# Performance work log

Hardware: AMD Instinct MI355X
Metric: run time of the kernel (lower is better)

The kernel has to match this reference:

```python
import jax, jax.numpy as jnp
import numpy as np

MEX_C = 2.0 / (np.sqrt(3.0) * np.pi ** 0.25)

def mexican_hat(z):
    return MEX_C * (z * z - 1.0) * jnp.exp(-0.5 * z * z)

def setup_inputs() -> dict:
    key = jax.random.key(0)
    ks = jax.random.split(key, 5)
    B, T, D, O = 4, 2048, 128, 128
    x = jax.random.normal(ks[0], (B, T, D), dtype=jnp.float32)
    # init like torch: scale ~ U(0.5,1.5), translation ~ U(-0.5,0.5), kaiming-ish weights
    scale = jax.random.uniform(ks[1], (O, D), dtype=jnp.float32, minval=0.5, maxval=1.5)
    translation = jax.random.uniform(ks[2], (O, D), dtype=jnp.float32, minval=-0.5, maxval=0.5)
    bound = 1.0 / np.sqrt(D)
    wavelet_weights = jax.random.uniform(ks[3], (O, D), dtype=jnp.float32, minval=-bound, maxval=bound)
    base_w = jax.random.uniform(ks[4], (O, D), dtype=jnp.float32, minval=-bound, maxval=bound)
    ln_gamma = jnp.ones((D,), dtype=jnp.float32)
    ln_beta = jnp.zeros((D,), dtype=jnp.float32)
    return {"x": x, "scale": scale, "translation": translation,
            "wavelet_weights": wavelet_weights, "base_w": base_w,
            "ln_gamma": ln_gamma, "ln_beta": ln_beta}

def reference(x, scale, translation, wavelet_weights, base_w, ln_gamma, ln_beta):
    B, T, D = x.shape
    O = wavelet_weights.shape[0]
    # LayerNorm over last dim (eps = 1e-5, torch default)
    mu = jnp.mean(x, axis=-1, keepdims=True)
    var = jnp.mean((x - mu) ** 2, axis=-1, keepdims=True)
    x_norm = (x - mu) / jnp.sqrt(var + 1e-5) * ln_gamma + ln_beta
    x_flat = x_norm.reshape(B * T, D)                      # (N, D)
    s = jax.nn.softplus(scale) + 0.1                       # (O, D)
    # broadcast intermediate (N, O, D) — the memory-bound path
    z = (x_flat[:, None, :] - translation[None]) / s[None]
    w = jnp.clip(mexican_hat(z), -10.0, 10.0)              # (N, O, D)
    wavelet_out = jnp.einsum('nod,od->no', w, wavelet_weights)
    base_out = x.reshape(B * T, D) @ base_w.T              # base uses raw x
    out = wavelet_out + jax.nn.silu(base_out)
    return out.reshape(B, T, O)
```

## Files before the change

kernel.cpp:

```cpp
#include <hip/hip_runtime.h>


#define D_DIM 128
#define O_DIM 128
#define ROWS  16
#define BLOCK 1024
#define CHUNK 16
#define NCHUNK (D_DIM / CHUNK)
#define XSTRIDE 9

#define C1     0.72134752f
#define SQRT_C 0.84932180f
#define WWK    1.2023651f
#define LOG2E  1.44269504f

typedef float v2f __attribute__((ext_vector_type(2)));

__global__ __launch_bounds__(256) void wavekan_prep(
    const float* __restrict__ scale,
    const float* __restrict__ trans,
    const float* __restrict__ ww,
    const float* __restrict__ bw,
    float4* __restrict__ wsW)
{
    int idx = blockIdx.x * blockDim.x + threadIdx.x;
    if (idx >= O_DIM * D_DIM) return;
    int o = idx >> 7;
    int d = idx & (D_DIM - 1);
    float sc = scale[idx];
    float sp = fmaxf(sc, 0.0f) + log1pf(__expf(-fabsf(sc)));
    float is2 = SQRT_C / (sp + 0.1f);
    float4 w;
    w.x = trans[idx] * is2;
    w.y = is2;
    w.z = ww[idx] * WWK;
    w.w = bw[idx];
    wsW[d * O_DIM + o] = w;
}

template<bool USE_WS>
__global__ __launch_bounds__(BLOCK, 8) void wavekan_main(
    const float* __restrict__ x,
    const float* __restrict__ scale,
    const float* __restrict__ trans,
    const float* __restrict__ ww,
    const float* __restrict__ bw,
    const float* __restrict__ gamma,
    const float* __restrict__ beta,
    const float4* __restrict__ wsW,
    float* __restrict__ out,
    int N)
{
    __shared__ float4 s_x[D_DIM * XSTRIDE];
    __shared__ float4 s_w[CHUNK * O_DIM];

    const int tid  = threadIdx.x;
    const int row0 = blockIdx.x * ROWS;

    {
        const int r  = tid >> 6;
        const int j  = tid & 63;
        const int d0 = j * 2;
        const int grow = row0 + r;

        float2 v2 = make_float2(0.f, 0.f);
        if (grow < N)
            v2 = *reinterpret_cast<const float2*>(x + (size_t)grow * D_DIM + d0);

        float sum = v2.x + v2.y;
        float ssq = v2.x * v2.x + v2.y * v2.y;
        #pragma unroll
        for (int m = 1; m < 64; m <<= 1) {
            sum += __shfl_xor(sum, m, 64);
            ssq += __shfl_xor(ssq, m, 64);
        }
        const float mean = sum * (1.0f / D_DIM);
        const float var  = ssq * (1.0f / D_DIM) - mean * mean;
        const float rstd = rsqrtf(var + 1e-5f);

        float2 g2 = *reinterpret_cast<const float2*>(gamma + d0);
        float2 b2 = *reinterpret_cast<const float2*>(beta + d0);

        const int p  = r >> 1;
        const int h  = r & 1;
        float* c0 = reinterpret_cast<float*>(&s_x[d0 * XSTRIDE + p]);
        float* c1 = reinterpret_cast<float*>(&s_x[(d0 + 1) * XSTRIDE + p]);
        c0[h]     = (v2.x - mean) * rstd * g2.x + b2.x;
        c0[2 + h] = v2.x;
        c1[h]     = (v2.y - mean) * rstd * g2.y + b2.y;
        c1[2 + h] = v2.y;
    }

    const int o = tid & (O_DIM - 1);
    const int g = tid >> 7;

    v2f accw = {0.f, 0.f};
    v2f accb = {0.f, 0.f};

    if (USE_WS) {
        float4 r0 = wsW[tid];
        float4 r1 = wsW[tid + BLOCK];
        for (int c = 0; c < NCHUNK; ++c) {
            __syncthreads();
            s_w[tid]         = r0;
            s_w[tid + BLOCK] = r1;
            if (c + 1 < NCHUNK) {
                r0 = wsW[(c + 1) * (CHUNK * O_DIM) + tid];
                r1 = wsW[(c + 1) * (CHUNK * O_DIM) + tid + BLOCK];
            }
            __syncthreads();

            #pragma unroll
            for (int dl = 0; dl < CHUNK; ++dl) {
                float4 w  = s_w[dl * O_DIM + o];
                float4 xx = s_x[(c * CHUNK + dl) * XSTRIDE + g];
                v2f xln = {xx.x, xx.y};
                v2f xrw = {xx.z, xx.w};
                v2f u   = xln * w.y - w.x;
                v2f q   = u * u;
                v2f s1  = q - C1;
                v2f e   = {__builtin_amdgcn_exp2f(-q.x),
                           __builtin_amdgcn_exp2f(-q.y)};
                accw += (s1 * e) * w.z;
                accb += xrw * w.w;
            }
        }
    } else {
        __syncthreads();
        for (int d = 0; d < D_DIM; ++d) {
            int idx = o * D_DIM + d;
            float sc = scale[idx];
            float sp = fmaxf(sc, 0.0f) + log1pf(__expf(-fabsf(sc)));
            float is  = SQRT_C / (sp + 0.1f);
            float tws = trans[idx] * is;
            float wwk = ww[idx] * WWK;
            float bwv = bw[idx];
            float4 xx = s_x[d * XSTRIDE + g];
            v2f xln = {xx.x, xx.y};
            v2f xrw = {xx.z, xx.w};
            v2f u   = xln * is - tws;
            v2f q   = u * u;
            v2f s1  = q - C1;
            v2f e   = {__builtin_amdgcn_exp2f(-q.x),
                       __builtin_amdgcn_exp2f(-q.y)};
            accw += (s1 * e) * wwk;
            accb += xrw * bwv;
        }
    }

    {
        const int rr0 = row0 + g * 2;
        if (rr0 < N) {
            float sig0 = 1.0f / (1.0f + __builtin_amdgcn_exp2f(-LOG2E * accb.x));
            out[(size_t)rr0 * O_DIM + o] = accw.x + accb.x * sig0;
        }
        if (rr0 + 1 < N) {
            float sig1 = 1.0f / (1.0f + __builtin_amdgcn_exp2f(-LOG2E * accb.y));
            out[(size_t)(rr0 + 1) * O_DIM + o] = accw.y + accb.y * sig1;
        }
    }
}

extern "C" void kernel_launch(void* const* d_in, const int* in_sizes, int n_in,
                              void* d_out, int out_size, void* d_ws, size_t ws_size,
                              hipStream_t stream) {
    const float* x     = (const float*)d_in[0];
    const float* scale = (const float*)d_in[1];
    const float* trans = (const float*)d_in[2];
    const float* ww    = (const float*)d_in[3];
    const float* bw    = (const float*)d_in[4];
    const float* gamma = (const float*)d_in[5];
    const float* beta  = (const float*)d_in[6];
    float* out = (float*)d_out;

    const int N = in_sizes[0] / D_DIM;
    const int grid = (N + ROWS - 1) / ROWS;

    const size_t ws_needed = (size_t)O_DIM * D_DIM * sizeof(float4);
    if (ws_size >= ws_needed) {
        wavekan_prep<<<(O_DIM * D_DIM + 255) / 256, 256, 0, stream>>>(
            scale, trans, ww, bw, (float4*)d_ws);
        wavekan_main<true><<<grid, BLOCK, 0, stream>>>(
            x, scale, trans, ww, bw, gamma, beta, (const float4*)d_ws, out, N);
    } else {
        wavekan_main<false><<<grid, BLOCK, 0, stream>>>(
            x, scale, trans, ww, bw, gamma, beta, nullptr, out, N);
    }
}
```

Before: 97.29 us.

## Fuse weight preprocessing into main kernel and drop separate prep launch

Removes the separate prep kernel that wrote transformed per-(o,d) parameters to workspace. Each block now loads the raw scale, translation and weights chunk by chunk, computes the softplus-derived terms in registers, and transposes them into shared memory, with the next chunk's loads and transform overlapped with compute. This saves a kernel launch and a workspace round trip. In exchange every block (512 of them) recomputes log1p/exp/div for the whole weight set, and the shared-memory store becomes strided.

```diff
diff --git a/kernel.cpp b/kernel.cpp
--- a/kernel.cpp
+++ b/kernel.cpp
@@ -16,29 +16,17 @@
 
 typedef float v2f __attribute__((ext_vector_type(2)));
 
-__global__ __launch_bounds__(256) void wavekan_prep(
-    const float* __restrict__ scale,
-    const float* __restrict__ trans,
-    const float* __restrict__ ww,
-    const float* __restrict__ bw,
-    float4* __restrict__ wsW)
-{
-    int idx = blockIdx.x * blockDim.x + threadIdx.x;
-    if (idx >= O_DIM * D_DIM) return;
-    int o = idx >> 7;
-    int d = idx & (D_DIM - 1);
-    float sc = scale[idx];
-    float sp = fmaxf(sc, 0.0f) + log1pf(__expf(-fabsf(sc)));
+__device__ __forceinline__ float4 wk_transform(float sc, float tr, float w_w, float b_w) {
+    float sp  = fmaxf(sc, 0.0f) + log1pf(__expf(-fabsf(sc)));
     float is2 = SQRT_C / (sp + 0.1f);
     float4 w;
-    w.x = trans[idx] * is2;
+    w.x = tr * is2;
     w.y = is2;
-    w.z = ww[idx] * WWK;
-    w.w = bw[idx];
-    wsW[d * O_DIM + o] = w;
+    w.z = w_w * WWK;
+    w.w = b_w;
+    return w;
 }
 
-template<bool USE_WS>
 __global__ __launch_bounds__(BLOCK, 8) void wavekan_main(
     const float* __restrict__ x,
     const float* __restrict__ scale,
@@ -47,7 +35,6 @@
     const float* __restrict__ bw,
     const float* __restrict__ gamma,
     const float* __restrict__ beta,
-    const float4* __restrict__ wsW,
     float* __restrict__ out,
     int N)
 {
@@ -91,60 +78,60 @@
         c1[2 + h] = v2.y;
     }
 
+    const int so    = tid >> 3;
+    const int sq    = tid & 7;
+    const int wbase = so * D_DIM + sq * 2;
+
+    float4 r0, r1;
+    {
+        float2 sc2 = *reinterpret_cast<const float2*>(scale + wbase);
+        float2 tr2 = *reinterpret_cast<const float2*>(trans + wbase);
+        float2 wv2 = *reinterpret_cast<const float2*>(ww    + wbase);
+        float2 bv2 = *reinterpret_cast<const float2*>(bw    + wbase);
+        r0 = wk_transform(sc2.x, tr2.x, wv2.x, bv2.x);
+        r1 = wk_transform(sc2.y, tr2.y, wv2.y, bv2.y);
+    }
+
     const int o = tid & (O_DIM - 1);
     const int g = tid >> 7;
 
     v2f accw = {0.f, 0.f};
     v2f accb = {0.f, 0.f};
 
-    if (USE_WS) {
-        float4 r0 = wsW[tid];
-        float4 r1 = wsW[tid + BLOCK];
-        for (int c = 0; c < NCHUNK; ++c) {
-            __syncthreads();
-            s_w[tid]         = r0;
-            s_w[tid + BLOCK] = r1;
-            if (c + 1 < NCHUNK) {
-                r0 = wsW[(c + 1) * (CHUNK * O_DIM) + tid];
-                r1 = wsW[(c + 1) * (CHUNK * O_DIM) + tid + BLOCK];
-            }
-            __syncthreads();
+    for (int c = 0; c < NCHUNK; ++c) {
+        __syncthreads();
+        s_w[(sq * 2)     * O_DIM + so] = r0;
+        s_w[(sq * 2 + 1) * O_DIM + so] = r1;
+        __syncthreads();
 
-            #pragma unroll
-            for (int dl = 0; dl < CHUNK; ++dl) {
-                float4 w  = s_w[dl * O_DIM + o];
-                float4 xx = s_x[(c * CHUNK + dl) * XSTRIDE + g];
-                v2f xln = {xx.x, xx.y};
-                v2f xrw = {xx.z, xx.w};
-                v2f u   = xln * w.y - w.x;
-                v2f q   = u * u;
-                v2f s1  = q - C1;
-                v2f e   = {__builtin_amdgcn_exp2f(-q.x),
-                           __builtin_amdgcn_exp2f(-q.y)};
-                accw += (s1 * e) * w.z;
-                accb += xrw * w.w;
-            }
+        float2 sc2, tr2, wv2, bv2;
+        const bool more = (c + 1 < NCHUNK);
+        if (more) {
+            const int off = wbase + (c + 1) * CHUNK;
+            sc2 = *reinterpret_cast<const float2*>(scale + off);
+            tr2 = *reinterpret_cast<const float2*>(trans + off);
+            wv2 = *reinterpret_cast<const float2*>(ww    + off);
+            bv2 = *reinterpret_cast<const float2*>(bw    + off);
         }
-    } else {
-        __syncthreads();
-        for (int d = 0; d < D_DIM; ++d) {
-            int idx = o * D_DIM + d;
-            float sc = scale[idx];
-            float sp = fmaxf(sc, 0.0f) + log1pf(__expf(-fabsf(sc)));
-            float is  = SQRT_C / (sp + 0.1f);
-            float tws = trans[idx] * is;
-            float wwk = ww[idx] * WWK;
-            float bwv = bw[idx];
-            float4 xx = s_x[d * XSTRIDE + g];
+
+        #pragma unroll
+        for (int dl = 0; dl < CHUNK; ++dl) {
+            float4 w  = s_w[dl * O_DIM + o];
+            float4 xx = s_x[(c * CHUNK + dl) * XSTRIDE + g];
             v2f xln = {xx.x, xx.y};
             v2f xrw = {xx.z, xx.w};
-            v2f u   = xln * is - tws;
+            v2f u   = xln * w.y - w.x;
             v2f q   = u * u;
             v2f s1  = q - C1;
             v2f e   = {__builtin_amdgcn_exp2f(-q.x),
                        __builtin_amdgcn_exp2f(-q.y)};
-            accw += (s1 * e) * wwk;
-            accb += xrw * bwv;
+            accw += (s1 * e) * w.z;
+            accb += xrw * w.w;
+        }
+
+        if (more) {
+            r0 = wk_transform(sc2.x, tr2.x, wv2.x, bv2.x);
+            r1 = wk_transform(sc2.y, tr2.y, wv2.y, bv2.y);
         }
     }
 
@@ -176,14 +163,8 @@
     const int N = in_sizes[0] / D_DIM;
     const int grid = (N + ROWS - 1) / ROWS;
 
-    const size_t ws_needed = (size_t)O_DIM * D_DIM * sizeof(float4);
-    if (ws_size >= ws_needed) {
-        wavekan_prep<<<(O_DIM * D_DIM + 255) / 256, 256, 0, stream>>>(
-            scale, trans, ww, bw, (float4*)d_ws);
-        wavekan_main<true><<<grid, BLOCK, 0, stream>>>(
-            x, scale, trans, ww, bw, gamma, beta, (const float4*)d_ws, out, N);
-    } else {
-        wavekan_main<false><<<grid, BLOCK, 0, stream>>>(
-            x, scale, trans, ww, bw, gamma, beta, nullptr, out, N);
-    }
+    (void)d_ws; (void)ws_size;
+
+    wavekan_main<<<grid, BLOCK, 0, stream>>>(
+        x, scale, trans, ww, bw, gamma, beta, out, N);
 }
```

After: 125.8 us. +29.3%, slower.
